# Performance work log

Measured on AMD Instinct MI355X. Metric: run time of the kernel, lower is better.

## Reference

```python
import jax, jax.numpy as jnp
import numpy as np


def fps(xyz, nsamples):
    # xyz: [B, N, 3] -> [B, nsamples] furthest-point-sample indices (int32)
    def single(p):
        N = p.shape[0]
        def step(carry, _):
            dists, last = carry
            d = jnp.sum((p - p[last]) ** 2, axis=-1)
            dists = jnp.minimum(dists, d)
            return (dists, jnp.argmax(dists).astype(jnp.int32)), last
        init = (jnp.full((N,), 1e10, p.dtype), jnp.int32(0))
        _, idx = jax.lax.scan(step, init, None, length=nsamples)
        return idx
    return jax.vmap(single)(xyz)


def bn_relu(x, g, b, m, v):
    # inference BatchNorm2d folded into scale/shift, then ReLU; x: [B,C,S,N]
    s = g * jax.lax.rsqrt(v + 1e-5)
    return jax.nn.relu(x * s[None, :, None, None] + (b - m * s)[None, :, None, None])


def setup_inputs() -> dict:
    key = jax.random.key(0)
    ks = jax.random.split(key, 6)
    B, N, C, S = 8, 16384, 64, 5
    return dict(
        fg_xyz=jax.random.normal(ks[0], (B, N, 3), jnp.float32),
        fg_features=jax.random.normal(ks[1], (B, C, N), jnp.float32),
        bg_xyz=jax.random.normal(ks[2], (B, N, 3), jnp.float32),
        bg_features=jax.random.normal(ks[3], (B, C, N), jnp.float32),
        w1=jax.random.normal(ks[4], (C, 2 * C), jnp.float32) * (1.0 / np.sqrt(2 * C)),
        g1=jnp.ones((C,), jnp.float32), b1=jnp.zeros((C,), jnp.float32),
        m1=jnp.zeros((C,), jnp.float32), v1=jnp.ones((C,), jnp.float32),
        w2=jax.random.normal(ks[5], (C, C), jnp.float32) * (1.0 / np.sqrt(C)),
        g2=jnp.ones((C,), jnp.float32), b2=jnp.zeros((C,), jnp.float32),
        m2=jnp.zeros((C,), jnp.float32), v2=jnp.ones((C,), jnp.float32),
        nsamples=5,
    )


def reference(fg_xyz, fg_features, bg_xyz, bg_features,
              w1, g1, b1, m1, v1, w2, g2, b2, m2, v2, nsamples):
    B, C, N = fg_features.shape
    S = nsamples
    # D-FPS sample S background points, gather their features: [B, C, S]
    idx = fps(bg_xyz, S)
    sample_bg = jnp.take_along_axis(
        bg_features, jnp.broadcast_to(idx[:, None, :], (B, C, S)), axis=2)
    fg_exp = fg_features[:, :, None, :]                           # [B, C, 1, N]
    # candidates = [fg itself, S sampled bg feats tiled over the N fg points]
    fused_origin = jnp.concatenate(
        [fg_exp, jnp.broadcast_to(sample_bg[:, :, :, None], (B, C, S, N))], axis=2)  # [B,C,S+1,N]
    # weight-net input: fg feature concatenated with each candidate along channels
    fusion_in = jnp.concatenate(
        [jnp.broadcast_to(fg_exp, (B, C, S + 1, N)), fused_origin], axis=1)          # [B,2C,S+1,N]
    h = bn_relu(jnp.einsum('oc,bcsn->bosn', w1, fusion_in), g1, b1, m1, v1)
    w = bn_relu(jnp.einsum('oc,bcsn->bosn', w2, h), g2, b2, m2, v2)                  # [B,C,S+1,N]
    final_feats = jnp.sum(w * fused_origin, axis=2, keepdims=True)                   # [B,C,1,N]
    return fg_xyz, final_feats
```

## Files before the change

### kernel.cpp

```cpp
#include <hip/hip_runtime.h>

#define B_ 8
#define N_ 16384
#define C_ 64
#define S_ 5

typedef float v4f __attribute__((ext_vector_type(4)));
typedef __bf16 v8bf __attribute__((ext_vector_type(8)));
typedef unsigned int v4u __attribute__((ext_vector_type(4)));

static __device__ __forceinline__ unsigned short f2bf(float f) {
    unsigned int u = __float_as_uint(f);
    u += 0x7fffu + ((u >> 16) & 1u);
    return (unsigned short)(u >> 16);
}
static __device__ __forceinline__ float bf2f(unsigned short s) {
    return __uint_as_float(((unsigned int)s) << 16);
}

__global__ __launch_bounds__(256) void prep_w_copy(
    const float* __restrict__ w1, const float* __restrict__ g1, const float* __restrict__ b1,
    const float* __restrict__ m1, const float* __restrict__ v1,
    const float* __restrict__ w2, const float* __restrict__ g2, const float* __restrict__ b2,
    const float* __restrict__ m2, const float* __restrict__ v2,
    float* __restrict__ w1bs, float* __restrict__ bb1, float* __restrict__ bb2,
    unsigned short* __restrict__ wa_bf, unsigned short* __restrict__ wc_bf,
    unsigned short* __restrict__ w2_bf,
    const float* __restrict__ fg_xyz, float* __restrict__ out_xyz) {
    const int t = threadIdx.x;
    const int blk = blockIdx.x;
    if (blk > 0) {
        const float4* src = (const float4*)(fg_xyz + (size_t)(blk - 1) * 4096);
        float4* dst = (float4*)(out_xyz + (size_t)(blk - 1) * 4096);
#pragma unroll
        for (int i = 0; i < 4; ++i) dst[t + i * 256] = src[t + i * 256];
        return;
    }
    for (int i = t; i < 64 * 64; i += 256) {
        const int o = i >> 6, c = i & 63;
        const float s1 = g1[o] / sqrtf(v1[o] + 1e-5f);
        const float s2 = g2[o] / sqrtf(v2[o] + 1e-5f);
        const float a = s1 * w1[o * 128 + c];
        const float bb = s1 * w1[o * 128 + 64 + c];
        w1bs[o * 64 + c] = bb;
        wa_bf[o * 64 + c] = f2bf(a);
        wc_bf[o * 64 + c] = f2bf(a + bb);
        w2_bf[o * 64 + c] = f2bf(s2 * w2[o * 64 + c]);
    }
    if (t < 64) {
        const float s1 = g1[t] / sqrtf(v1[t] + 1e-5f);
        const float s2 = g2[t] / sqrtf(v2[t] + 1e-5f);
        bb1[t] = b1[t] - m1[t] * s1;
        bb2[t] = b2[t] - m2[t] * s2;
    }
}

__global__ __launch_bounds__(512) void fps_sbg(
    const float* __restrict__ xyz, const float* __restrict__ bg_feat,
    const float* __restrict__ w1bs, const float* __restrict__ bb1,
    float* __restrict__ sbg, float* __restrict__ ebb) {
    const int b = blockIdx.x;
    const float* p = xyz + (size_t)b * N_ * 3;
    const int t = threadIdx.x;
    const int PPT = N_ / 512;

    float px[PPT], py[PPT], pz[PPT], dist[PPT];
#pragma unroll
    for (int k = 0; k < PPT; ++k) {
        int i = t + k * 512;
        px[k] = p[i * 3 + 0];
        py[k] = p[i * 3 + 1];
        pz[k] = p[i * 3 + 2];
        dist[k] = 1e10f;
    }

    __shared__ float s_best[8];
    __shared__ int s_bidx[8];
    __shared__ int s_last;
    __shared__ int s_idx[S_];
    __shared__ float sf[S_][64];
    int last = 0;
    if (t == 0) s_idx[0] = 0;

    for (int step = 1; step < S_; ++step) {
        const float lx = p[last * 3 + 0];
        const float ly = p[last * 3 + 1];
        const float lz = p[last * 3 + 2];
        float best = -1.0f;
        int bidx = 0;
#pragma unroll
        for (int k = 0; k < PPT; ++k) {
            float dx = px[k] - lx, dy = py[k] - ly, dz = pz[k] - lz;
            float d = dx * dx + dy * dy + dz * dz;
            float nd = fminf(dist[k], d);
            dist[k] = nd;
            if (nd > best) { best = nd; bidx = t + k * 512; }
        }
#pragma unroll
        for (int off = 32; off > 0; off >>= 1) {
            float ob = __shfl_down(best, off, 64);
            int oi = __shfl_down(bidx, off, 64);
            if (ob > best || (ob == best && oi < bidx)) { best = ob; bidx = oi; }
        }
        if ((t & 63) == 0) { s_best[t >> 6] = best; s_bidx[t >> 6] = bidx; }
        __syncthreads();
        if (t == 0) {
            float bb = s_best[0];
            int bi = s_bidx[0];
#pragma unroll
            for (int w = 1; w < 8; ++w) {
                if (s_best[w] > bb || (s_best[w] == bb && s_bidx[w] < bi)) {
                    bb = s_best[w];
                    bi = s_bidx[w];
                }
            }
            s_last = bi;
            s_idx[step] = bi;
        }
        __syncthreads();
        last = s_last;
        __syncthreads();
    }

    if (t < S_ * 64) {
        const int j = t >> 6, c = t & 63;
        sf[j][c] = bg_feat[(size_t)b * C_ * N_ + (size_t)c * N_ + s_idx[j]];
    }
    __syncthreads();
    if (t < S_ * 64) {
        const int j = t >> 6, o = t & 63;
        const float4* wr = (const float4*)&w1bs[o * 64];
        float acc = 0.f;
#pragma unroll
        for (int c4 = 0; c4 < 16; ++c4) {
            float4 wv = wr[c4];
            acc += wv.x * sf[j][c4 * 4 + 0] + wv.y * sf[j][c4 * 4 + 1] +
                   wv.z * sf[j][c4 * 4 + 2] + wv.w * sf[j][c4 * 4 + 3];
        }
        sbg[(b * S_ + j) * 64 + o] = sf[j][o];
        ebb[(b * S_ + j) * 64 + o] = acc + bb1[o];
    }
}

#define PITCH 72

__global__ __launch_bounds__(256) void fusion_main(
    const float* __restrict__ fg_feat,
    const unsigned short* __restrict__ wa_bf, const unsigned short* __restrict__ wc_bf,
    const unsigned short* __restrict__ w2_bf,
    const float* __restrict__ bb1g, const float* __restrict__ bb2g,
    const float* __restrict__ ebbg, const float* __restrict__ sbgg,
    float* __restrict__ out) {
    __shared__ __align__(16) unsigned short Ft[64 * PITCH];
    __shared__ __align__(16) unsigned short Ht[2][4][16 * PITCH];
    __shared__ __align__(16) float cEbb[S_ * 64];
    __shared__ __align__(16) float cSbg[S_ * 64];
    __shared__ __align__(16) float cBb1[64];
    __shared__ __align__(16) float cBb2[64];

    const int t = threadIdx.x;
    const int b = blockIdx.y;
    const int n0 = blockIdx.x * 64;
    const float* Fg = fg_feat + (size_t)b * C_ * N_ + n0;

    {
        const int n = t & 63;
        const int cg = (t >> 6) * 16;
        v4u w0, w1v;
#pragma unroll
        for (int i = 0; i < 8; ++i) {
            unsigned short lo = f2bf(Fg[(size_t)(cg + 2 * i) * N_ + n]);
            unsigned short hi = f2bf(Fg[(size_t)(cg + 2 * i + 1) * N_ + n]);
            unsigned int packed = (unsigned int)lo | ((unsigned int)hi << 16);
            if (i < 4) w0[i] = packed; else w1v[i - 4] = packed;
        }
        *(v4u*)&Ft[n * PITCH + cg] = w0;
        *(v4u*)&Ft[n * PITCH + cg + 8] = w1v;
    }
    for (int i = t; i < S_ * 64; i += 256) {
        cEbb[i] = ebbg[b * (S_ * 64) + i];
        cSbg[i] = sbgg[b * (S_ * 64) + i];
    }
    if (t < 64) { cBb1[t] = bb1g[t]; cBb2[t] = bb2g[t]; }

    const int lane = t & 63;
    const int w = t >> 6;
    const int m = lane & 15;
    const int q = lane >> 4;
    const int nrow = w * 16 + m;

    v8bf aWa[4][2], aWc[4][2], aW2[4][2];
#pragma unroll
    for (int ob = 0; ob < 4; ++ob)
#pragma unroll
        for (int ks = 0; ks < 2; ++ks) {
            const int widx = (ob * 16 + m) * 64 + ks * 32 + q * 8;
            aWa[ob][ks] = *(const v8bf*)&wa_bf[widx];
            aWc[ob][ks] = *(const v8bf*)&wc_bf[widx];
            aW2[ob][ks] = *(const v8bf*)&w2_bf[widx];
        }

    __syncthreads();

    v8bf bF[2];
#pragma unroll
    for (int ks = 0; ks < 2; ++ks)
        bF[ks] = *(const v8bf*)&Ft[nrow * PITCH + ks * 32 + q * 8];

    v4f U[4], U0[4];
#pragma unroll
    for (int ob = 0; ob < 4; ++ob) {
        v4f z = {0.f, 0.f, 0.f, 0.f};
        z = __builtin_amdgcn_mfma_f32_16x16x32_bf16(aWa[ob][0], bF[0], z, 0, 0, 0);
        U[ob] = __builtin_amdgcn_mfma_f32_16x16x32_bf16(aWa[ob][1], bF[1], z, 0, 0, 0);
        v4f z2 = {0.f, 0.f, 0.f, 0.f};
        z2 = __builtin_amdgcn_mfma_f32_16x16x32_bf16(aWc[ob][0], bF[0], z2, 0, 0, 0);
        U0[ob] = __builtin_amdgcn_mfma_f32_16x16x32_bf16(aWc[ob][1], bF[1], z2, 0, 0, 0);
    }

    v4f acc[4];
#pragma unroll
    for (int ob = 0; ob < 4; ++ob) acc[ob] = (v4f){0.f, 0.f, 0.f, 0.f};

#pragma unroll
    for (int s = 0; s < 6; ++s) {
        unsigned short* h = &Ht[s & 1][w][0];

#pragma unroll
        for (int ob = 0; ob < 4; ++ob) {
            const int o4 = ob * 16 + 4 * q;
            v4f cv, u;
            if (s == 0) { cv = *(const v4f*)&cBb1[o4]; u = U0[ob]; }
            else        { cv = *(const v4f*)&cEbb[(s - 1) * 64 + o4]; u = U[ob]; }
            unsigned int lo = (unsigned int)f2bf(fmaxf(u[0] + cv[0], 0.f)) |
                              ((unsigned int)f2bf(fmaxf(u[1] + cv[1], 0.f)) << 16);
            unsigned int hi = (unsigned int)f2bf(fmaxf(u[2] + cv[2], 0.f)) |
                              ((unsigned int)f2bf(fmaxf(u[3] + cv[3], 0.f)) << 16);
            unsigned long long v = (unsigned long long)lo | ((unsigned long long)hi << 32);
            *(unsigned long long*)&h[m * PITCH + o4] = v;
        }

        v8bf hb0 = *(const v8bf*)&h[m * PITCH + q * 8];
        v8bf hb1 = *(const v8bf*)&h[m * PITCH + 32 + q * 8];

#pragma unroll
        for (int ob = 0; ob < 4; ++ob) {
            v4f z = {0.f, 0.f, 0.f, 0.f};
            z = __builtin_amdgcn_mfma_f32_16x16x32_bf16(aW2[ob][0], hb0, z, 0, 0, 0);
            v4f p = __builtin_amdgcn_mfma_f32_16x16x32_bf16(aW2[ob][1], hb1, z, 0, 0, 0);

            const int o4 = ob * 16 + 4 * q;
            const v4f b2v = *(const v4f*)&cBb2[o4];
            if (s == 0) {
                unsigned long long fv = *(const unsigned long long*)&Ft[nrow * PITCH + o4];
#pragma unroll
                for (int r = 0; r < 4; ++r) {
                    float wgt = fmaxf(p[r] + b2v[r], 0.f);
                    acc[ob][r] += wgt * bf2f((unsigned short)(fv >> (16 * r)));
                }
            } else {
                const v4f sb = *(const v4f*)&cSbg[(s - 1) * 64 + o4];
#pragma unroll
                for (int r = 0; r < 4; ++r) {
                    float wgt = fmaxf(p[r] + b2v[r], 0.f);
                    acc[ob][r] += wgt * sb[r];
                }
            }
        }
    }

#pragma unroll
    for (int ob = 0; ob < 4; ++ob)
#pragma unroll
        for (int r = 0; r < 4; ++r)
            out[(size_t)b * C_ * N_ + (size_t)(ob * 16 + 4 * q + r) * N_ + (n0 + w * 16 + m)] =
                acc[ob][r];
}

extern "C" void kernel_launch(void* const* d_in, const int* in_sizes, int n_in,
                              void* d_out, int out_size, void* d_ws, size_t ws_size,
                              hipStream_t stream) {
    const float* fg_xyz = (const float*)d_in[0];
    const float* fg_feat = (const float*)d_in[1];
    const float* bg_xyz = (const float*)d_in[2];
    const float* bg_feat = (const float*)d_in[3];
    const float* w1 = (const float*)d_in[4];
    const float* g1 = (const float*)d_in[5];
    const float* b1 = (const float*)d_in[6];
    const float* m1 = (const float*)d_in[7];
    const float* v1 = (const float*)d_in[8];
    const float* w2 = (const float*)d_in[9];
    const float* g2 = (const float*)d_in[10];
    const float* b2 = (const float*)d_in[11];
    const float* m2 = (const float*)d_in[12];
    const float* v2 = (const float*)d_in[13];

    float* ws = (float*)d_ws;
    float* w1bs = ws;
    float* ebb = w1bs + 4096;
    float* sbg = ebb + 2560;
    float* bb1 = sbg + 2560;
    float* bb2 = bb1 + 64;
    unsigned short* wa_bf = (unsigned short*)(bb2 + 64);
    unsigned short* wc_bf = wa_bf + 4096;
    unsigned short* w2_bf = wc_bf + 4096;

    float* out_feats = (float*)d_out + (size_t)B_ * N_ * 3;

    prep_w_copy<<<97, 256, 0, stream>>>(w1, g1, b1, m1, v1, w2, g2, b2, m2, v2,
                                        w1bs, bb1, bb2, wa_bf, wc_bf, w2_bf,
                                        fg_xyz, (float*)d_out);
    fps_sbg<<<B_, 512, 0, stream>>>(bg_xyz, bg_feat, w1bs, bb1, sbg, ebb);
    fusion_main<<<dim3(N_ / 64, B_), 256, 0, stream>>>(
        fg_feat, wa_bf, wc_bf, w2_bf, bb1, bb2, ebb, sbg, out_feats);
}
```

Measured before the change: 174.7 us.

## Merge prep and FPS kernels; load fg features straight to LDS asynchronously

Folds weight preparation, the xyz copy and furthest-point sampling into one 1024-thread launch. The FPS now reads contiguous float4 xyz chunks per thread, and the sampled-background bias term is computed directly from w1, which removes one kernel launch and the dependency between the first two kernels. In the main kernel, fg features go from global memory into LDS as fp32 via global_load_lds, are converted to bf16 on read, and the Wa/Wc weights are loaded where they are used instead of held in registers. The main risks are extra LDS traffic, bank conflicts on strided fp32 reads, and the FPS running with a different thread and index layout.

Result: no change. 178.0 us (+1.9%).

```diff
diff --git a/kernel.cpp b/kernel.cpp
--- a/kernel.cpp
+++ b/kernel.cpp
@@ -1,4 +1,5 @@
 #include <hip/hip_runtime.h>
+#include <hip/hip_bf16.h>
 
 #define B_ 8
 #define N_ 16384
@@ -7,75 +8,76 @@
 
 typedef float v4f __attribute__((ext_vector_type(4)));
 typedef __bf16 v8bf __attribute__((ext_vector_type(8)));
-typedef unsigned int v4u __attribute__((ext_vector_type(4)));
 
 static __device__ __forceinline__ unsigned short f2bf(float f) {
     unsigned int u = __float_as_uint(f);
     u += 0x7fffu + ((u >> 16) & 1u);
     return (unsigned short)(u >> 16);
 }
-static __device__ __forceinline__ float bf2f(unsigned short s) {
-    return __uint_as_float(((unsigned int)s) << 16);
-}
-
-__global__ __launch_bounds__(256) void prep_w_copy(
+
+#define GETF(A, i) (((i) & 3) == 0 ? A[(i) >> 2].x : ((i) & 3) == 1 ? A[(i) >> 2].y \
+                    : ((i) & 3) == 2 ? A[(i) >> 2].z : A[(i) >> 2].w)
+
+__global__ __launch_bounds__(1024, 4) void prep_all(
+    const float* __restrict__ bg_xyz, const float* __restrict__ bg_feat,
     const float* __restrict__ w1, const float* __restrict__ g1, const float* __restrict__ b1,
     const float* __restrict__ m1, const float* __restrict__ v1,
     const float* __restrict__ w2, const float* __restrict__ g2, const float* __restrict__ b2,
     const float* __restrict__ m2, const float* __restrict__ v2,
-    float* __restrict__ w1bs, float* __restrict__ bb1, float* __restrict__ bb2,
+    const float* __restrict__ fg_xyz, float* __restrict__ out_xyz,
+    float* __restrict__ bb1, float* __restrict__ bb2,
     unsigned short* __restrict__ wa_bf, unsigned short* __restrict__ wc_bf,
     unsigned short* __restrict__ w2_bf,
-    const float* __restrict__ fg_xyz, float* __restrict__ out_xyz) {
+    float* __restrict__ sbg, float* __restrict__ ebb) {
+    const int blk = blockIdx.x;
     const int t = threadIdx.x;
-    const int blk = blockIdx.x;
-    if (blk > 0) {
-        const float4* src = (const float4*)(fg_xyz + (size_t)(blk - 1) * 4096);
-        float4* dst = (float4*)(out_xyz + (size_t)(blk - 1) * 4096);
-#pragma unroll
-        for (int i = 0; i < 4; ++i) dst[t + i * 256] = src[t + i * 256];
+
+    if (blk >= 9) {
+        const int i = (blk - 9) * 1024 + t;
+        ((float4*)out_xyz)[i] = ((const float4*)fg_xyz)[i];
         return;
     }
-    for (int i = t; i < 64 * 64; i += 256) {
-        const int o = i >> 6, c = i & 63;
-        const float s1 = g1[o] / sqrtf(v1[o] + 1e-5f);
-        const float s2 = g2[o] / sqrtf(v2[o] + 1e-5f);
-        const float a = s1 * w1[o * 128 + c];
-        const float bb = s1 * w1[o * 128 + 64 + c];
-        w1bs[o * 64 + c] = bb;
-        wa_bf[o * 64 + c] = f2bf(a);
-        wc_bf[o * 64 + c] = f2bf(a + bb);
-        w2_bf[o * 64 + c] = f2bf(s2 * w2[o * 64 + c]);
-    }
-    if (t < 64) {
-        const float s1 = g1[t] / sqrtf(v1[t] + 1e-5f);
-        const float s2 = g2[t] / sqrtf(v2[t] + 1e-5f);
-        bb1[t] = b1[t] - m1[t] * s1;
-        bb2[t] = b2[t] - m2[t] * s2;
-    }
-}
-
-__global__ __launch_bounds__(512) void fps_sbg(
-    const float* __restrict__ xyz, const float* __restrict__ bg_feat,
-    const float* __restrict__ w1bs, const float* __restrict__ bb1,
-    float* __restrict__ sbg, float* __restrict__ ebb) {
-    const int b = blockIdx.x;
-    const float* p = xyz + (size_t)b * N_ * 3;
-    const int t = threadIdx.x;
-    const int PPT = N_ / 512;
-
-    float px[PPT], py[PPT], pz[PPT], dist[PPT];
-#pragma unroll
-    for (int k = 0; k < PPT; ++k) {
-        int i = t + k * 512;
-        px[k] = p[i * 3 + 0];
-        py[k] = p[i * 3 + 1];
-        pz[k] = p[i * 3 + 2];
+
+    if (blk == 8) {
+        for (int i = t; i < 64 * 64; i += 1024) {
+            const int o = i >> 6, c = i & 63;
+            const float s1 = g1[o] / sqrtf(v1[o] + 1e-5f);
+            const float s2 = g2[o] / sqrtf(v2[o] + 1e-5f);
+            const float a = s1 * w1[o * 128 + c];
+            const float bbv = s1 * w1[o * 128 + 64 + c];
+            wa_bf[o * 64 + c] = f2bf(a);
+            wc_bf[o * 64 + c] = f2bf(a + bbv);
+            w2_bf[o * 64 + c] = f2bf(s2 * w2[o * 64 + c]);
+        }
+        if (t < 64) {
+            const float s1 = g1[t] / sqrtf(v1[t] + 1e-5f);
+            const float s2 = g2[t] / sqrtf(v2[t] + 1e-5f);
+            bb1[t] = b1[t] - m1[t] * s1;
+            bb2[t] = b2[t] - m2[t] * s2;
+        }
+        return;
+    }
+
+    const int b = blk;
+    const float* p = bg_xyz + (size_t)b * N_ * 3;
+
+    float4 f4[12];
+    {
+        const float4* pv = (const float4*)p + t * 12;
+#pragma unroll
+        for (int i = 0; i < 12; ++i) f4[i] = pv[i];
+    }
+    float px[16], py[16], pz[16], dist[16];
+#pragma unroll
+    for (int k = 0; k < 16; ++k) {
+        px[k] = GETF(f4, 3 * k);
+        py[k] = GETF(f4, 3 * k + 1);
+        pz[k] = GETF(f4, 3 * k + 2);
         dist[k] = 1e10f;
     }
 
-    __shared__ float s_best[8];
-    __shared__ int s_bidx[8];
+    __shared__ float s_best[16];
+    __shared__ int s_bidx[16];
     __shared__ int s_last;
     __shared__ int s_idx[S_];
     __shared__ float sf[S_][64];
@@ -89,12 +91,12 @@
         float best = -1.0f;
         int bidx = 0;
 #pragma unroll
-        for (int k = 0; k < PPT; ++k) {
+        for (int k = 0; k < 16; ++k) {
             float dx = px[k] - lx, dy = py[k] - ly, dz = pz[k] - lz;
             float d = dx * dx + dy * dy + dz * dz;
             float nd = fminf(dist[k], d);
             dist[k] = nd;
-            if (nd > best) { best = nd; bidx = t + k * 512; }
+            if (nd > best) { best = nd; bidx = t * 16 + k; }
         }
 #pragma unroll
         for (int off = 32; off > 0; off >>= 1) {
@@ -108,7 +110,7 @@
             float bb = s_best[0];
             int bi = s_bidx[0];
 #pragma unroll
-            for (int w = 1; w < 8; ++w) {
+            for (int w = 1; w < 16; ++w) {
                 if (s_best[w] > bb || (s_best[w] == bb && s_bidx[w] < bi)) {
                     bb = s_best[w];
                     bi = s_bidx[w];
@@ -122,6 +124,7 @@
         __syncthreads();
     }
 
+    __syncthreads();
     if (t < S_ * 64) {
         const int j = t >> 6, c = t & 63;
         sf[j][c] = bg_feat[(size_t)b * C_ * N_ + (size_t)c * N_ + s_idx[j]];
@@ -129,7 +132,8 @@
     __syncthreads();
     if (t < S_ * 64) {
         const int j = t >> 6, o = t & 63;
-        const float4* wr = (const float4*)&w1bs[o * 64];
+        const float s1 = g1[o] * rsqrtf(v1[o] + 1e-5f);
+        const float4* wr = (const float4*)&w1[o * 128 + 64];
         float acc = 0.f;
 #pragma unroll
         for (int c4 = 0; c4 < 16; ++c4) {
@@ -138,11 +142,12 @@
                    wv.z * sf[j][c4 * 4 + 2] + wv.w * sf[j][c4 * 4 + 3];
         }
         sbg[(b * S_ + j) * 64 + o] = sf[j][o];
-        ebb[(b * S_ + j) * 64 + o] = acc + bb1[o];
+        ebb[(b * S_ + j) * 64 + o] = s1 * acc + (b1[o] - m1[o] * s1);
     }
 }
 
-#define PITCH 72
+#define FP 64
+#define HP 72
 
 __global__ __launch_bounds__(256) void fusion_main(
     const float* __restrict__ fg_feat,
@@ -151,8 +156,8 @@
     const float* __restrict__ bb1g, const float* __restrict__ bb2g,
     const float* __restrict__ ebbg, const float* __restrict__ sbgg,
     float* __restrict__ out) {
-    __shared__ __align__(16) unsigned short Ft[64 * PITCH];
-    __shared__ __align__(16) unsigned short Ht[2][4][16 * PITCH];
+    __shared__ __align__(16) float Flds[64 * FP];
+    __shared__ __align__(16) unsigned short Ht[2][4][16 * HP];
     __shared__ __align__(16) float cEbb[S_ * 64];
     __shared__ __align__(16) float cSbg[S_ * 64];
     __shared__ __align__(16) float cBb1[64];
@@ -163,59 +168,71 @@
     const int n0 = blockIdx.x * 64;
     const float* Fg = fg_feat + (size_t)b * C_ * N_ + n0;
 
+    const int lane = t & 63;
+    const int w = t >> 6;
+
     {
-        const int n = t & 63;
-        const int cg = (t >> 6) * 16;
-        v4u w0, w1v;
-#pragma unroll
-        for (int i = 0; i < 8; ++i) {
-            unsigned short lo = f2bf(Fg[(size_t)(cg + 2 * i) * N_ + n]);
-            unsigned short hi = f2bf(Fg[(size_t)(cg + 2 * i + 1) * N_ + n]);
-            unsigned int packed = (unsigned int)lo | ((unsigned int)hi << 16);
-            if (i < 4) w0[i] = packed; else w1v[i - 4] = packed;
-        }
-        *(v4u*)&Ft[n * PITCH + cg] = w0;
-        *(v4u*)&Ft[n * PITCH + cg + 8] = w1v;
-    }
+        const int crow = lane >> 4;
+        const int nq = lane & 15;
+#pragma unroll
+        for (int r = 0; r < 4; ++r) {
+            const int c = r * 16 + w * 4;
+            const float* gsrc = Fg + (size_t)(c + crow) * N_ + nq * 4;
+            __builtin_amdgcn_global_load_lds(
+                (const __attribute__((address_space(1))) unsigned int*)gsrc,
+                (__attribute__((address_space(3))) unsigned int*)&Flds[c * FP],
+                16, 0, 0);
+        }
+    }
+
     for (int i = t; i < S_ * 64; i += 256) {
         cEbb[i] = ebbg[b * (S_ * 64) + i];
         cSbg[i] = sbgg[b * (S_ * 64) + i];
     }
     if (t < 64) { cBb1[t] = bb1g[t]; cBb2[t] = bb2g[t]; }
 
-    const int lane = t & 63;
-    const int w = t >> 6;
     const int m = lane & 15;
     const int q = lane >> 4;
     const int nrow = w * 16 + m;
 
-    v8bf aWa[4][2], aWc[4][2], aW2[4][2];
+    v8bf aW2[4][2];
 #pragma unroll
     for (int ob = 0; ob < 4; ++ob)
 #pragma unroll
-        for (int ks = 0; ks < 2; ++ks) {
-            const int widx = (ob * 16 + m) * 64 + ks * 32 + q * 8;
-            aWa[ob][ks] = *(const v8bf*)&wa_bf[widx];
-            aWc[ob][ks] = *(const v8bf*)&wc_bf[widx];
-            aW2[ob][ks] = *(const v8bf*)&w2_bf[widx];
-        }
+        for (int ks = 0; ks < 2; ++ks)
+            aW2[ob][ks] = *(const v8bf*)&w2_bf[(ob * 16 + m) * 64 + ks * 32 + q * 8];
 
     __syncthreads();
 
     v8bf bF[2];
 #pragma unroll
-    for (int ks = 0; ks < 2; ++ks)
-        bF[ks] = *(const v8bf*)&Ft[nrow * PITCH + ks * 32 + q * 8];
+    for (int ks = 0; ks < 2; ++ks) {
+        unsigned int uu[4];
+#pragma unroll
+        for (int jp = 0; jp < 4; ++jp) {
+            const int c = ks * 32 + q * 8 + jp * 2;
+            float2 fp2;
+            fp2.x = Flds[c * FP + nrow];
+            fp2.y = Flds[(c + 1) * FP + nrow];
+            __hip_bfloat162 h2 = __float22bfloat162_rn(fp2);
+            __builtin_memcpy(&uu[jp], &h2, 4);
+        }
+        __builtin_memcpy(&bF[ks], uu, 16);
+    }
 
     v4f U[4], U0[4];
 #pragma unroll
     for (int ob = 0; ob < 4; ++ob) {
+        v8bf a0 = *(const v8bf*)&wa_bf[(ob * 16 + m) * 64 + q * 8];
+        v8bf a1 = *(const v8bf*)&wa_bf[(ob * 16 + m) * 64 + 32 + q * 8];
         v4f z = {0.f, 0.f, 0.f, 0.f};
-        z = __builtin_amdgcn_mfma_f32_16x16x32_bf16(aWa[ob][0], bF[0], z, 0, 0, 0);
-        U[ob] = __builtin_amdgcn_mfma_f32_16x16x32_bf16(aWa[ob][1], bF[1], z, 0, 0, 0);
+        z = __builtin_amdgcn_mfma_f32_16x16x32_bf16(a0, bF[0], z, 0, 0, 0);
+        U[ob] = __builtin_amdgcn_mfma_f32_16x16x32_bf16(a1, bF[1], z, 0, 0, 0);
+        v8bf c0 = *(const v8bf*)&wc_bf[(ob * 16 + m) * 64 + q * 8];
+        v8bf c1 = *(const v8bf*)&wc_bf[(ob * 16 + m) * 64 + 32 + q * 8];
         v4f z2 = {0.f, 0.f, 0.f, 0.f};
-        z2 = __builtin_amdgcn_mfma_f32_16x16x32_bf16(aWc[ob][0], bF[0], z2, 0, 0, 0);
-        U0[ob] = __builtin_amdgcn_mfma_f32_16x16x32_bf16(aWc[ob][1], bF[1], z2, 0, 0, 0);
+        z2 = __builtin_amdgcn_mfma_f32_16x16x32_bf16(c0, bF[0], z2, 0, 0, 0);
+        U0[ob] = __builtin_amdgcn_mfma_f32_16x16x32_bf16(c1, bF[1], z2, 0, 0, 0);
     }
 
     v4f acc[4];
@@ -229,40 +246,45 @@
 #pragma unroll
         for (int ob = 0; ob < 4; ++ob) {
             const int o4 = ob * 16 + 4 * q;
-            v4f cv, u;
-            if (s == 0) { cv = *(const v4f*)&cBb1[o4]; u = U0[ob]; }
-            else        { cv = *(const v4f*)&cEbb[(s - 1) * 64 + o4]; u = U[ob]; }
-            unsigned int lo = (unsigned int)f2bf(fmaxf(u[0] + cv[0], 0.f)) |
-                              ((unsigned int)f2bf(fmaxf(u[1] + cv[1], 0.f)) << 16);
-            unsigned int hi = (unsigned int)f2bf(fmaxf(u[2] + cv[2], 0.f)) |
-                              ((unsigned int)f2bf(fmaxf(u[3] + cv[3], 0.f)) << 16);
-            unsigned long long v = (unsigned long long)lo | ((unsigned long long)hi << 32);
-            *(unsigned long long*)&h[m * PITCH + o4] = v;
-        }
-
-        v8bf hb0 = *(const v8bf*)&h[m * PITCH + q * 8];
-        v8bf hb1 = *(const v8bf*)&h[m * PITCH + 32 + q * 8];
+            v4f u, cv;
+            if (s == 0) { u = U0[ob]; cv = *(const v4f*)&cBb1[o4]; }
+            else        { u = U[ob];  cv = *(const v4f*)&cEbb[(s - 1) * 64 + o4]; }
+            float2 e01, e23;
+            e01.x = fmaxf(u[0] + cv[0], 0.f);
+            e01.y = fmaxf(u[1] + cv[1], 0.f);
+            e23.x = fmaxf(u[2] + cv[2], 0.f);
+            e23.y = fmaxf(u[3] + cv[3], 0.f);
+            __hip_bfloat162 h01 = __float22bfloat162_rn(e01);
+            __hip_bfloat162 h23 = __float22bfloat162_rn(e23);
+            unsigned int lo, hi;
+            __builtin_memcpy(&lo, &h01, 4);
+            __builtin_memcpy(&hi, &h23, 4);
+            unsigned long long vv = (unsigned long long)lo | ((unsigned long long)hi << 32);
+            *(unsigned long long*)&h[m * HP + o4] = vv;
+        }
+
+        v8bf hb0 = *(const v8bf*)&h[m * HP + q * 8];
+        v8bf hb1 = *(const v8bf*)&h[m * HP + 32 + q * 8];
 
 #pragma unroll
         for (int ob = 0; ob < 4; ++ob) {
             v4f z = {0.f, 0.f, 0.f, 0.f};
             z = __builtin_amdgcn_mfma_f32_16x16x32_bf16(aW2[ob][0], hb0, z, 0, 0, 0);
-            v4f p = __builtin_amdgcn_mfma_f32_16x16x32_bf16(aW2[ob][1], hb1, z, 0, 0, 0);
+            v4f p4 = __builtin_amdgcn_mfma_f32_16x16x32_bf16(aW2[ob][1], hb1, z, 0, 0, 0);
 
             const int o4 = ob * 16 + 4 * q;
             const v4f b2v = *(const v4f*)&cBb2[o4];
             if (s == 0) {
-                unsigned long long fv = *(const unsigned long long*)&Ft[nrow * PITCH + o4];
 #pragma unroll
                 for (int r = 0; r < 4; ++r) {
-                    float wgt = fmaxf(p[r] + b2v[r], 0.f);
-                    acc[ob][r] += wgt * bf2f((unsigned short)(fv >> (16 * r)));
+                    float wgt = fmaxf(p4[r] + b2v[r], 0.f);
+                    acc[ob][r] += wgt * Flds[(o4 + r) * FP + nrow];
                 }
             } else {
                 const v4f sb = *(const v4f*)&cSbg[(s - 1) * 64 + o4];
 #pragma unroll
                 for (int r = 0; r < 4; ++r) {
-                    float wgt = fmaxf(p[r] + b2v[r], 0.f);
+                    float wgt = fmaxf(p4[r] + b2v[r], 0.f);
                     acc[ob][r] += wgt * sb[r];
                 }
             }
@@ -296,8 +318,7 @@
     const float* v2 = (const float*)d_in[13];
 
     float* ws = (float*)d_ws;
-    float* w1bs = ws;
-    float* ebb = w1bs + 4096;
+    float* ebb = ws;
     float* sbg = ebb + 2560;
     float* bb1 = sbg + 2560;
     float* bb2 = bb1 + 64;
@@ -307,10 +328,10 @@
 
     float* out_feats = (float*)d_out + (size_t)B_ * N_ * 3;
 
-    prep_w_copy<<<97, 256, 0, stream>>>(w1, g1, b1, m1, v1, w2, g2, b2, m2, v2,
-                                        w1bs, bb1, bb2, wa_bf, wc_bf, w2_bf,
-                                        fg_xyz, (float*)d_out);
-    fps_sbg<<<B_, 512, 0, stream>>>(bg_xyz, bg_feat, w1bs, bb1, sbg, ebb);
+    prep_all<<<105, 1024, 0, stream>>>(bg_xyz, bg_feat,
+                                       w1, g1, b1, m1, v1, w2, g2, b2, m2, v2,
+                                       fg_xyz, (float*)d_out,
+                                       bb1, bb2, wa_bf, wc_bf, w2_bf, sbg, ebb);
     fusion_main<<<dim3(N_ / 64, B_), 256, 0, stream>>>(
         fg_feat, wa_bf, wc_bf, w2_bf, bb1, bb2, ebb, sbg, out_feats);
 }
```
